# Optimization experiments

Measured on AMD Instinct MI355X. Metric: run time of the kernel, lower is better.

The kernel has to match this reference:

```python
import jax, jax.numpy as jnp
import numpy as np

DOF = 7
B = 8192
DT = 0.1
ACTION_RANGE = 50.0
MAX_VEL = 20.0


def _skew(w):
    x, y, z = w[..., 0], w[..., 1], w[..., 2]
    O = jnp.zeros_like(x)
    return jnp.stack([jnp.stack([O, -z, y], -1),
                      jnp.stack([z, O, -x], -1),
                      jnp.stack([-y, x, O], -1)], -2)


def _exp_se3(xi):
    # xi: (..., 6) twist [w; v] (already scaled by joint angle) -> (..., 4, 4)
    w, v = xi[..., :3], xi[..., 3:]
    th = jnp.sqrt(jnp.sum(w * w, -1))
    small = th < 1e-4
    ths = jnp.where(small, 1.0, th)  # safe denominator
    th2 = th * th
    a = jnp.where(small, 1.0 - th2 / 6.0, jnp.sin(th) / ths)
    b = jnp.where(small, 0.5 - th2 / 24.0, (1.0 - jnp.cos(th)) / (ths * ths))
    c = jnp.where(small, 1.0 / 6.0 - th2 / 120.0, (th - jnp.sin(th)) / (ths * ths * ths))
    K = _skew(w)
    K2 = K @ K
    I3 = jnp.eye(3, dtype=xi.dtype)
    R = I3 + a[..., None, None] * K + b[..., None, None] * K2
    Vm = I3 + b[..., None, None] * K + c[..., None, None] * K2
    p = jnp.einsum('...ij,...j->...i', Vm, v)
    top = jnp.concatenate([R, p[..., None]], -1)
    bot = jnp.broadcast_to(jnp.array([0.0, 0.0, 0.0, 1.0], xi.dtype), top.shape[:-2] + (1, 4))
    return jnp.concatenate([top, bot], -2)


def _inv_T(T):
    R = T[..., :3, :3]
    p = T[..., :3, 3]
    Rt = jnp.swapaxes(R, -1, -2)
    pn = -jnp.einsum('...ij,...j->...i', Rt, p)
    top = jnp.concatenate([Rt, pn[..., None]], -1)
    bot = jnp.broadcast_to(jnp.array([0.0, 0.0, 0.0, 1.0], T.dtype), top.shape[:-2] + (1, 4))
    return jnp.concatenate([top, bot], -2)


def _adjoint(T):
    # SE(3) adjoint for [w; v] twists: [[R, 0], [ [p]x R, R ]]
    R = T[..., :3, :3]
    p = T[..., :3, 3]
    pR = _skew(p) @ R
    Z = jnp.zeros_like(R)
    return jnp.concatenate([jnp.concatenate([R, Z], -1),
                            jnp.concatenate([pR, R], -1)], -2)


def _ad(V):
    # se(3) little adjoint: [[ [w]x, 0 ], [ [v]x, [w]x ]]
    Kw = _skew(V[..., :3])
    Kv = _skew(V[..., 3:])
    Z = jnp.zeros_like(Kw)
    return jnp.concatenate([jnp.concatenate([Kw, Z], -1),
                            jnp.concatenate([Kv, Kw], -1)], -2)


def _inverse_dynamics(q, dq, ddq, g, Ftip, M, G, A):
    # Recursive Newton-Euler (Modern Robotics, link-frame screws A).
    Bq, n = q.shape
    V = jnp.zeros((Bq, 6), q.dtype)
    Vd = jnp.broadcast_to(jnp.concatenate([jnp.zeros(3, q.dtype), -g]), (Bq, 6))
    AdTs, Vs, Vds = [], [], []
    for i in range(n):
        T = _exp_se3(-A[i] * q[:, i, None]) @ _inv_T(M[i])  # T_{i,i-1}, (B,4,4)
        AdT = _adjoint(T)
        V = jnp.einsum('bij,bj->bi', AdT, V) + A[i] * dq[:, i, None]
        Vd = (jnp.einsum('bij,bj->bi', AdT, Vd)
              + jnp.einsum('bij,j->bi', _ad(V), A[i]) * dq[:, i, None]
              + A[i] * ddq[:, i, None])
        AdTs.append(AdT)
        Vs.append(V)
        Vds.append(Vd)
    F = jnp.broadcast_to(Ftip.astype(q.dtype), (Bq, 6))
    AdT_end = _adjoint(_inv_T(M[n]))  # T_{n+1,n}, (6,6)
    taus = [None] * n
    for i in range(n - 1, -1, -1):
        if i == n - 1:
            F = jnp.einsum('ji,bj->bi', AdT_end, F)
        else:
            F = jnp.einsum('bji,bj->bi', AdTs[i + 1], F)
        F = (F + jnp.einsum('ij,bj->bi', G[i], Vds[i])
             - jnp.einsum('bji,jk,bk->bi', _ad(Vs[i]), G[i], Vs[i]))
        taus[i] = jnp.einsum('bi,i->b', F, A[i])
    return jnp.stack(taus, -1)  # (B, n)


def _forward_dynamics(q, dq, tau, g, Ftip, M, G, A):
    n = q.shape[1]
    zer = jnp.zeros_like(q)
    # bias forces: Coriolis + gravity + end-effector wrench
    h = _inverse_dynamics(q, dq, zer, g, Ftip, M, G, A)
    g0 = jnp.zeros(3, q.dtype)
    f0 = jnp.zeros(6, q.dtype)
    # mass matrix columns via unit accelerations (vmapped over columns)
    cols = jax.vmap(lambda e: _inverse_dynamics(
        q, zer, jnp.broadcast_to(e, q.shape), g0, f0, M, G, A))(jnp.eye(n, dtype=q.dtype))
    Mmat = jnp.transpose(cols, (1, 2, 0))  # (B, n, n)
    return jnp.linalg.solve(Mmat, (tau - h)[..., None])[..., 0]


def _fk_in_space(q, M, A):
    Bq, n = q.shape
    T = jnp.broadcast_to(jnp.eye(4, dtype=q.dtype), (Bq, 4, 4))
    outs = []
    for i in range(n):
        T = (T @ M[i]) @ _exp_se3(A[i] * q[:, i, None])
        outs.append(T)
    outs.append(T @ M[n])
    return jnp.stack(outs, 1)  # (B, n+1, 4, 4)


def setup_inputs():
    key = jax.random.key(0)
    ks = jax.random.split(key, 4)
    state = jax.random.normal(ks[0], (B, 2 * DOF), jnp.float32)
    torque = jax.random.normal(ks[1], (B, DOF), jnp.float32)
    M = jnp.tile(jnp.eye(4, dtype=jnp.float32)[None], (DOF + 1, 1, 1))
    A = jax.random.uniform(ks[2], (DOF, 6), jnp.float32)
    L = jax.random.normal(ks[3], (DOF, 6, 6), jnp.float32)
    gravity = jnp.array([0.0, -9.8, 0.0], jnp.float32)
    ftip = jnp.zeros(6, jnp.float32)
    return {"state": state, "torque": torque, "M": M, "A": A, "L": L,
            "gravity": gravity, "ftip": ftip}


def reference(state, torque, M, A, L, gravity, ftip):
    n = DOF
    G = L @ jnp.swapaxes(L, -1, -2)  # spatial inertias, PSD
    s0 = jnp.concatenate([state, torque * ACTION_RANGE], -1)  # (B, 3n)

    def derivs(s):
        q = s[..., :n]
        dq = s[..., n:2 * n]
        qf = s[..., 2 * n:]
        qacc = _forward_dynamics(q, dq, qf, gravity, ftip, M, G, A)
        return jnp.concatenate([dq, qacc, jnp.zeros_like(qf)], -1)

    k1 = derivs(s0)
    k2 = derivs(s0 + 0.5 * DT * k1)
    k3 = derivs(s0 + 0.5 * DT * k2)
    k4 = derivs(s0 + DT * k3)
    s1 = s0 + (DT / 6.0) * (k1 + 2.0 * k2 + 2.0 * k3 + k4)
    q = jnp.mod(s1[..., :n] + jnp.pi, 2.0 * jnp.pi) - jnp.pi
    dq = jnp.clip(s1[..., n:2 * n], -MAX_VEL, MAX_VEL)
    ee = _fk_in_space(q, M, A)
    return jnp.concatenate([q, dq], -1), ee[:, -1, :2, 3]
```

## Files before the change

kernel.cpp:

```cpp
#include <hip/hip_runtime.h>
#include <hip/hip_bf16.h>

#define DTC 0.1f
#define ACTION_RANGE 50.0f
#define MAX_VEL 20.0f
#define PI_F 3.14159265358979323846f
#define TWO_PI_F 6.28318530717958647692f
#define INV_TWO_PI_F 0.15915494309189533577f

__device__ __forceinline__ float bf2f(__hip_bfloat16 x){ return __bfloat162float(x); }
__device__ __forceinline__ float frcp(float x){ return __builtin_amdgcn_rcpf(x); }

__device__ __forceinline__ float ldv(const void* p, int i, bool isb){
  return isb ? __bfloat162float(((const __hip_bfloat16*)p)[i]) : ((const float*)p)[i];
}
__device__ __forceinline__ void stv(void* p, int i, float v, bool isb){
  if (isb) ((__hip_bfloat16*)p)[i] = __float2bfloat16(v);
  else     ((float*)p)[i] = v;
}

__device__ __forceinline__ void exp_se3_Rp(const float* Aj, float s, float* R, float* P){
  float wx=Aj[0]*s, wy=Aj[1]*s, wz=Aj[2]*s;
  float vx=Aj[3]*s, vy=Aj[4]*s, vz=Aj[5]*s;
  float th2 = wx*wx+wy*wy+wz*wz;
  float th = sqrtf(th2);
  float th4 = th2*th2;
  float aS = 1.f - th2*(1.f/6.f)  + th4*(1.f/120.f);
  float bS = 0.5f - th2*(1.f/24.f) + th4*(1.f/720.f);
  float cS = (1.f/6.f) - th2*(1.f/120.f) + th4*(1.f/5040.f);
  float sn = __sinf(th), cs = __cosf(th);
  float inv = frcp(th), inv2 = inv*inv;
  float aL = sn*inv;
  float bL = (1.f-cs)*inv2;
  float cL = (th-sn)*inv2*inv;
  bool sm = th < 0.25f;
  float a = sm?aS:aL, b = sm?bS:bL, c = sm?cS:cL;
  R[0]=1.f+b*(wx*wx-th2); R[1]=b*wx*wy-a*wz;      R[2]=b*wx*wz+a*wy;
  R[3]=b*wx*wy+a*wz;      R[4]=1.f+b*(wy*wy-th2); R[5]=b*wy*wz-a*wx;
  R[6]=b*wx*wz-a*wy;      R[7]=b*wy*wz+a*wx;      R[8]=1.f+b*(wz*wz-th2);
  float V0=1.f+c*(wx*wx-th2), V1=c*wx*wy-b*wz,      V2=c*wx*wz+b*wy;
  float V3=c*wx*wy+b*wz,      V4=1.f+c*(wy*wy-th2), V5=c*wy*wz-b*wx;
  float V6=c*wx*wz-b*wy,      V7=c*wy*wz+b*wx,      V8=1.f+c*(wz*wz-th2);
  P[0]=V0*vx+V1*vy+V2*vz;
  P[1]=V3*vx+V4*vy+V5*vz;
  P[2]=V6*vx+V7*vy+V8*vz;
}

__device__ __forceinline__ void mul33(const float* X, const float* Y, float* Z){
  #pragma unroll
  for (int r=0;r<3;r++){
    float x0=X[r*3+0], x1=X[r*3+1], x2=X[r*3+2];
    Z[r*3+0]=x0*Y[0]+x1*Y[3]+x2*Y[6];
    Z[r*3+1]=x0*Y[1]+x1*Y[4]+x2*Y[7];
    Z[r*3+2]=x0*Y[2]+x1*Y[5]+x2*Y[8];
  }
}

__device__ __forceinline__ void ad_apply(const float* R, const float* p, const float* Vin, float* Vout){
  float i0=Vin[0],i1=Vin[1],i2=Vin[2],i3=Vin[3],i4=Vin[4],i5=Vin[5];
  float w0 = R[0]*i0+R[1]*i1+R[2]*i2;
  float w1 = R[3]*i0+R[4]*i1+R[5]*i2;
  float w2 = R[6]*i0+R[7]*i1+R[8]*i2;
  float r0 = R[0]*i3+R[1]*i4+R[2]*i5;
  float r1 = R[3]*i3+R[4]*i4+R[5]*i5;
  float r2 = R[6]*i3+R[7]*i4+R[8]*i5;
  float p0=p[0],p1=p[1],p2=p[2];
  Vout[0]=w0; Vout[1]=w1; Vout[2]=w2;
  Vout[3]=p1*w2-p2*w1+r0;
  Vout[4]=p2*w0-p0*w2+r1;
  Vout[5]=p0*w1-p1*w0+r2;
}

__device__ __forceinline__ void adT_apply(const float* R, const float* p, const float* Fin, float* Fout){
  float m0=Fin[0],m1=Fin[1],m2=Fin[2],f0=Fin[3],f1=Fin[4],f2=Fin[5];
  float p0=p[0],p1=p[1],p2=p[2];
  float cx = m0 - (p1*f2 - p2*f1);
  float cy = m1 - (p2*f0 - p0*f2);
  float cz = m2 - (p0*f1 - p1*f0);
  float o0 = R[0]*cx + R[3]*cy + R[6]*cz;
  float o1 = R[1]*cx + R[4]*cy + R[7]*cz;
  float o2 = R[2]*cx + R[5]*cy + R[8]*cz;
  float o3 = R[0]*f0 + R[3]*f1 + R[6]*f2;
  float o4 = R[1]*f0 + R[4]*f1 + R[7]*f2;
  float o5 = R[2]*f0 + R[5]*f1 + R[8]*f2;
  Fout[0]=o0;Fout[1]=o1;Fout[2]=o2;Fout[3]=o3;Fout[4]=o4;Fout[5]=o5;
}

__device__ __forceinline__ void gmatvec2_sym(const float* Gu, const float* v, const float* d,
                                             float* gv, float* gvd){
  float g0=Gu[0],g1=Gu[1],g2=Gu[2],g3=Gu[3],g4=Gu[4],g5=Gu[5];
  float g6=Gu[6],g7=Gu[7],g8=Gu[8],g9=Gu[9],g10=Gu[10];
  float g11=Gu[11],g12=Gu[12],g13=Gu[13],g14=Gu[14];
  float g15=Gu[15],g16=Gu[16],g17=Gu[17],g18=Gu[18],g19=Gu[19],g20=Gu[20];
  gv[0]=g0*v[0]+g1 *v[1]+g2 *v[2]+g3 *v[3]+g4 *v[4]+g5 *v[5];
  gv[1]=g1*v[0]+g6 *v[1]+g7 *v[2]+g8 *v[3]+g9 *v[4]+g10*v[5];
  gv[2]=g2*v[0]+g7 *v[1]+g11*v[2]+g12*v[3]+g13*v[4]+g14*v[5];
  gv[3]=g3*v[0]+g8 *v[1]+g12*v[2]+g15*v[3]+g16*v[4]+g17*v[5];
  gv[4]=g4*v[0]+g9 *v[1]+g13*v[2]+g16*v[3]+g18*v[4]+g19*v[5];
  gv[5]=g5*v[0]+g10*v[1]+g14*v[2]+g17*v[3]+g19*v[4]+g20*v[5];
  gvd[0]=g0*d[0]+g1 *d[1]+g2 *d[2]+g3 *d[3]+g4 *d[4]+g5 *d[5];
  gvd[1]=g1*d[0]+g6 *d[1]+g7 *d[2]+g8 *d[3]+g9 *d[4]+g10*d[5];
  gvd[2]=g2*d[0]+g7 *d[1]+g11*d[2]+g12*d[3]+g13*d[4]+g14*d[5];
  gvd[3]=g3*d[0]+g8 *d[1]+g12*d[2]+g15*d[3]+g16*d[4]+g17*d[5];
  gvd[4]=g4*d[0]+g9 *d[1]+g13*d[2]+g16*d[3]+g18*d[4]+g19*d[5];
  gvd[5]=g5*d[0]+g10*d[1]+g14*d[2]+g17*d[3]+g19*d[4]+g20*d[5];
}

#define W_STRIDE 100

__global__ __launch_bounds__(64) void arm_rk4_kernel(
    const void* __restrict__ g_state,
    const void* __restrict__ g_torque,
    const void* __restrict__ g_M,
    const void* __restrict__ g_A,
    const void* __restrict__ g_L,
    const void* __restrict__ g_grav,
    const void* __restrict__ g_ftip,
    void* __restrict__ g_out,
    int B)
{
  __shared__ __align__(16) float sA8[56];
  __shared__ __align__(16) float sGu[168];
  __shared__ float sMinvR[72];
  __shared__ float sMinvp[24];
  __shared__ float sMR[72];
  __shared__ float sMp[24];
  __shared__ float sgrav[3];
  __shared__ float sftip[6];
  __shared__ __align__(16) float sW[8*W_STRIDE];
  __shared__ float sacc_lds[7*6*64];
  __shared__ float m_lds[7*64];
  __shared__ float dqs_lds[7*8];

  const bool isb = fabsf(bf2f(((const __hip_bfloat16*)g_grav)[1]) + 9.8f) < 0.5f;

  const int t = threadIdx.x;
  for (int x=t; x<56; x+=64){
    int i = x >> 3, k = x & 7;
    sA8[x] = (k < 6) ? ldv(g_A, i*6+k, isb) : 0.f;
  }
  for (int x=t; x<168; x+=64){
    int i = x/24; int u = x - i*24;
    if (u < 21){
      int rr = 0, u2 = u;
      while (u2 >= 6-rr){ u2 -= 6-rr; rr++; }
      int cc = rr + u2;
      float s = 0.f;
      #pragma unroll
      for (int k=0;k<6;k++) s += ldv(g_L, i*36+rr*6+k, isb) * ldv(g_L, i*36+cc*6+k, isb);
      sGu[x] = s;
    } else sGu[x] = 0.f;
  }
  if (t < 8){
    float R[9], p[3];
    #pragma unroll
    for (int rr=0;rr<3;rr++){
      #pragma unroll
      for (int cc=0;cc<3;cc++) R[rr*3+cc] = ldv(g_M, t*16 + rr*4 + cc, isb);
      p[rr] = ldv(g_M, t*16 + rr*4 + 3, isb);
    }
    #pragma unroll
    for (int rr=0;rr<3;rr++){
      #pragma unroll
      for (int cc=0;cc<3;cc++){ sMR[t*9+rr*3+cc] = R[rr*3+cc]; sMinvR[t*9+rr*3+cc] = R[cc*3+rr]; }
      sMp[t*3+rr] = p[rr];
      sMinvp[t*3+rr] = -(R[0*3+rr]*p[0] + R[1*3+rr]*p[1] + R[2*3+rr]*p[2]);
    }
  }
  if (t == 0){ for (int k=0;k<3;k++) sgrav[k] = ldv(g_grav, k, isb); }
  if (t == 1){ for (int k=0;k<6;k++) sftip[k] = ldv(g_ftip, k, isb); }
  __syncthreads();

  const int e = t >> 3;
  const int r = t & 7;
  int b = blockIdx.x * 8 + e;
  if (b >= B) b = B - 1;
  const bool is7 = (r == 7);
  float* W = &sW[e*W_STRIDE];

  float q0[7], dq0[7], qf[7];
  #pragma unroll
  for (int i=0;i<7;i++){
    q0[i]  = ldv(g_state, b*14+i, isb);
    dq0[i] = ldv(g_state, b*14+7+i, isb);
    qf[i]  = ldv(g_torque, b*7+i, isb) * ACTION_RANGE;
  }
  float kq[7], kdd[7], accq[7], accdq[7];
  #pragma unroll
  for (int i=0;i<7;i++){ kq[i]=0.f; kdd[i]=0.f; accq[i]=0.f; accdq[i]=0.f; }

  float Fend[6];
  {
    float tf[6]; adT_apply(&sMinvR[63], &sMinvp[21], sftip, tf);
    #pragma unroll
    for (int k=0;k<6;k++) Fend[k] = is7 ? tf[k] : 0.f;
  }

  #pragma unroll 1
  for (int st=0; st<4; ++st){
    const float cin = (st==0) ? 0.f : ((st==3) ? DTC : 0.5f*DTC);
    const float wgt = (st==0||st==3) ? (DTC/6.f) : (DTC/3.f);
    float qs[7], dqs[7];
    #pragma unroll
    for (int i=0;i<7;i++){ qs[i]=q0[i]+cin*kq[i]; dqs[i]=dq0[i]+cin*kdd[i]; }

    float qsr = 0.f;
    #pragma unroll
    for (int c=0;c<7;c++) qsr = (r==c) ? qs[c] : qsr;

    if (is7){
      #pragma unroll
      for (int i=0;i<7;i++) dqs_lds[i*8+e] = dqs[i];
    }

    if (r < 7){
      float Re[9], Pe[3], Rt[9];
      exp_se3_Rp(&sA8[r*8], -qsr, Re, Pe);
      mul33(Re, &sMinvR[r*9], Rt);
      float Tw[12];
      #pragma unroll
      for (int k=0;k<9;k++) Tw[k] = Rt[k];
      #pragma unroll
      for (int rr=0;rr<3;rr++)
        Tw[9+rr] = Re[rr*3+0]*sMinvp[r*3+0] + Re[rr*3+1]*sMinvp[r*3+1]
                 + Re[rr*3+2]*sMinvp[r*3+2] + Pe[rr];
      #pragma unroll
      for (int k=0;k<12;k++) W[r*12+k] = Tw[k];
    }
    __syncthreads();

    float V[6] = {0,0,0,0,0,0};
    float Vd[6];
    Vd[0]=0.f; Vd[1]=0.f; Vd[2]=0.f;
    Vd[3] = is7 ? -sgrav[0] : 0.f;
    Vd[4] = is7 ? -sgrav[1] : 0.f;
    Vd[5] = is7 ? -sgrav[2] : 0.f;
    #pragma unroll 1
    for (int i=0;i<7;i++){
      float Tl[12];
      #pragma unroll
      for (int k=0;k<12;k++) Tl[k] = W[i*12+k];
      float Al[6];
      #pragma unroll
      for (int k=0;k<6;k++) Al[k] = sA8[i*8+k];
      float dqi  = is7 ? dqs_lds[i*8+e] : 0.f;
      float ddqi = (!is7 && r==i) ? 1.f : 0.f;
      ad_apply(Tl, Tl+9, V, V);
      #pragma unroll
      for (int k=0;k<6;k++) V[k] += Al[k]*dqi;
      ad_apply(Tl, Tl+9, Vd, Vd);
      {
        float w0=V[0],w1=V[1],w2=V[2],v0=V[3],v1=V[4],v2=V[5];
        Vd[0] += (w1*Al[2]-w2*Al[1])*dqi + Al[0]*ddqi;
        Vd[1] += (w2*Al[0]-w0*Al[2])*dqi + Al[1]*ddqi;
        Vd[2] += (w0*Al[1]-w1*Al[0])*dqi + Al[2]*ddqi;
        Vd[3] += ((v1*Al[2]-v2*Al[1])+(w1*Al[5]-w2*Al[4]))*dqi + Al[3]*ddqi;
        Vd[4] += ((v2*Al[0]-v0*Al[2])+(w2*Al[3]-w0*Al[5]))*dqi + Al[4]*ddqi;
        Vd[5] += ((v0*Al[1]-v1*Al[0])+(w0*Al[4]-w1*Al[3]))*dqi + Al[5]*ddqi;
      }
      float gv[6], gvd[6];
      gmatvec2_sym(&sGu[i*24], V, Vd, gv, gvd);
      {
        float w0=V[0],w1=V[1],w2=V[2],v0=V[3],v1=V[4],v2=V[5];
        float s0 = gvd[0] + (w1*gv[2]-w2*gv[1]) + (v1*gv[5]-v2*gv[4]);
        float s1 = gvd[1] + (w2*gv[0]-w0*gv[2]) + (v2*gv[3]-v0*gv[5]);
        float s2 = gvd[2] + (w0*gv[1]-w1*gv[0]) + (v0*gv[4]-v1*gv[3]);
        float s3 = gvd[3] + (w1*gv[5]-w2*gv[4]);
        float s4 = gvd[4] + (w2*gv[3]-w0*gv[5]);
        float s5 = gvd[5] + (w0*gv[4]-w1*gv[3]);
        sacc_lds[(i*6+0)*64+t] = s0;
        sacc_lds[(i*6+1)*64+t] = s1;
        sacc_lds[(i*6+2)*64+t] = s2;
        sacc_lds[(i*6+3)*64+t] = s3;
        sacc_lds[(i*6+4)*64+t] = s4;
        sacc_lds[(i*6+5)*64+t] = s5;
      }
    }
    __syncthreads();

    {
      float F[6];
      #pragma unroll
      for (int k=0;k<6;k++) F[k] = Fend[k];
      #pragma unroll 1
      for (int i=6;i>=0;i--){
        if (i<6){
          float Tl[12];
          #pragma unroll
          for (int k=0;k<12;k++) Tl[k] = W[(i+1)*12+k];
          adT_apply(Tl, Tl+9, F, F);
        }
        #pragma unroll
        for (int k=0;k<6;k++) F[k] += sacc_lds[(i*6+k)*64+t];
        float Al[6];
        #pragma unroll
        for (int k=0;k<6;k++) Al[k] = sA8[i*8+k];
        m_lds[i*64+t] = F[0]*Al[0]+F[1]*Al[1]+F[2]*Al[2]
                      + F[3]*Al[3]+F[4]*Al[4]+F[5]*Al[5];
      }
    }
    __syncthreads();

    float U[7][7];
    #pragma unroll
    for (int i=0;i<7;i++){
      #pragma unroll
      for (int j=i;j<7;j++) U[i][j] = m_lds[j*64 + e*8 + i];
    }
    float rv[7];
    #pragma unroll
    for (int i=0;i<7;i++) rv[i] = qf[i] - m_lds[i*64 + e*8 + 7];
    #pragma unroll
    for (int k=0;k<7;k++){
      float dinv = frcp(U[k][k]);
      #pragma unroll
      for (int i=k+1;i<7;i++){
        float f = U[k][i]*dinv;
        #pragma unroll
        for (int j=i;j<7;j++) U[i][j] -= f*U[k][j];
        rv[i] -= f*rv[k];
      }
    }
    float x[7];
    #pragma unroll
    for (int i=6;i>=0;i--){
      float s = rv[i];
      #pragma unroll
      for (int j=i+1;j<7;j++) s -= U[i][j]*x[j];
      x[i] = s*frcp(U[i][i]);
    }

    #pragma unroll
    for (int i=0;i<7;i++){
      kq[i]  = dqs[i];
      kdd[i] = x[i];
      accq[i]  += wgt*dqs[i];
      accdq[i] += wgt*x[i];
    }
    __syncthreads();
  }

  float q1r=0.f, dq1r=0.f;
  #pragma unroll
  for (int c=0;c<7;c++){
    float xx = q0[c] + accq[c] + PI_F;
    float mm = xx - floorf(xx * INV_TWO_PI_F) * TWO_PI_F;
    float qv = mm - PI_F;
    float dv = dq0[c] + accdq[c];
    dv = fminf(fmaxf(dv, -MAX_VEL), MAX_VEL);
    q1r  = (r==c) ? qv : q1r;
    dq1r = (r==c) ? dv : dq1r;
  }

  {
    float XR[9], Xp[3];
    if (r < 7){
      float Re[9], Pe[3];
      exp_se3_Rp(&sA8[r*8], q1r, Re, Pe);
      mul33(&sMR[r*9], Re, XR);
      #pragma unroll
      for (int rr=0;rr<3;rr++)
        Xp[rr] = sMR[r*9+rr*3+0]*Pe[0]+sMR[r*9+rr*3+1]*Pe[1]+sMR[r*9+rr*3+2]*Pe[2] + sMp[r*3+rr];
    } else {
      #pragma unroll
      for (int k=0;k<9;k++) XR[k] = sMR[63+k];
      #pragma unroll
      for (int k=0;k<3;k++) Xp[k] = sMp[21+k];
    }
    #pragma unroll
    for (int k=0;k<9;k++) W[r*12+k]   = XR[k];
    #pragma unroll
    for (int k=0;k<3;k++) W[r*12+9+k] = Xp[k];
  }
  __syncthreads();

  #pragma unroll
  for (int w=4; w>=1; w>>=1){
    float Ra[9], pa[3], Rb[9], pb[3];
    if (r < w){
      #pragma unroll
      for (int k=0;k<9;k++){ Ra[k]=W[(2*r)*12+k]; Rb[k]=W[(2*r+1)*12+k]; }
      #pragma unroll
      for (int k=0;k<3;k++){ pa[k]=W[(2*r)*12+9+k]; pb[k]=W[(2*r+1)*12+9+k]; }
    }
    __syncthreads();
    if (r < w){
      float Rc[9];
      mul33(Ra, Rb, Rc);
      #pragma unroll
      for (int k=0;k<9;k++) W[r*12+k] = Rc[k];
      #pragma unroll
      for (int rr=0;rr<3;rr++)
        W[r*12+9+rr] = Ra[rr*3+0]*pb[0]+Ra[rr*3+1]*pb[1]+Ra[rr*3+2]*pb[2] + pa[rr];
    }
    __syncthreads();
  }

  if (r < 7){
    stv(g_out, b*14+r,   q1r,  isb);
    stv(g_out, b*14+7+r, dq1r, isb);
  } else {
    stv(g_out, B*14 + b*2 + 0, W[9],  isb);
    stv(g_out, B*14 + b*2 + 1, W[10], isb);
  }
}

extern "C" void kernel_launch(void* const* d_in, const int* in_sizes, int n_in,
                              void* d_out, int out_size, void* d_ws, size_t ws_size,
                              hipStream_t stream) {
  const int B = in_sizes[0] / 14;
  const int blocks = (B + 7) / 8;
  arm_rk4_kernel<<<blocks, 64, 0, stream>>>(d_in[0], d_in[1], d_in[2], d_in[3],
                                            d_in[4], d_in[5], d_in[6], d_out, B);
}
```

Baseline: 96.47 us.

## Keep per-lane RK4 state in scalars, drop redundant barriers, unroll RNEA loops

Each lane now carries only its own joint's q, dq, stage derivative and RK4 accumulators as scalars instead of full 7-element arrays. Only the is7 lane keeps a 7-wide copy of the previous solution, which it needs to publish dqs to LDS. The change also removes the barrier between the forward and backward Newton-Euler passes, since each thread reads back its own sacc entries, and removes the barrier at the end of each RK stage. The forward and backward link loops are unrolled by two. The aim is to cut register pressure, select chains and barrier stalls. The risk is that the barrier removal depends on subtle LDS ordering between stages.

```diff
diff --git a/kernel.cpp b/kernel.cpp
--- a/kernel.cpp
+++ b/kernel.cpp
@@ -178,16 +178,22 @@
   const bool is7 = (r == 7);
   float* W = &sW[e*W_STRIDE];
 
-  float q0[7], dq0[7], qf[7];
+  float dq0[7], qf[7];
   #pragma unroll
   for (int i=0;i<7;i++){
-    q0[i]  = ldv(g_state, b*14+i, isb);
     dq0[i] = ldv(g_state, b*14+7+i, isb);
     qf[i]  = ldv(g_torque, b*7+i, isb) * ACTION_RANGE;
   }
-  float kq[7], kdd[7], accq[7], accdq[7];
+  float q0r = ldv(g_state, b*14 + (is7 ? 0 : r), isb);
+  float dq0r = 0.f;
   #pragma unroll
-  for (int i=0;i<7;i++){ kq[i]=0.f; kdd[i]=0.f; accq[i]=0.f; accdq[i]=0.f; }
+  for (int c=0;c<7;c++) dq0r = (r==c) ? dq0[c] : dq0r;
+
+  float px[7];
+  #pragma unroll
+  for (int i=0;i<7;i++) px[i] = 0.f;
+  float pxr = 0.f, pdqr = 0.f;
+  float accq_r = 0.f, accdq_r = 0.f;
 
   float Fend[6];
   {
@@ -200,17 +206,12 @@
   for (int st=0; st<4; ++st){
     const float cin = (st==0) ? 0.f : ((st==3) ? DTC : 0.5f*DTC);
     const float wgt = (st==0||st==3) ? (DTC/6.f) : (DTC/3.f);
-    float qs[7], dqs[7];
-    #pragma unroll
-    for (int i=0;i<7;i++){ qs[i]=q0[i]+cin*kq[i]; dqs[i]=dq0[i]+cin*kdd[i]; }
-
-    float qsr = 0.f;
-    #pragma unroll
-    for (int c=0;c<7;c++) qsr = (r==c) ? qs[c] : qsr;
+    const float dqsr = dq0r + cin*pxr;
+    const float qsr  = q0r  + cin*pdqr;
 
     if (is7){
       #pragma unroll
-      for (int i=0;i<7;i++) dqs_lds[i*8+e] = dqs[i];
+      for (int i=0;i<7;i++) dqs_lds[i*8+e] = dq0[i] + cin*px[i];
     }
 
     if (r < 7){
@@ -235,7 +236,7 @@
     Vd[3] = is7 ? -sgrav[0] : 0.f;
     Vd[4] = is7 ? -sgrav[1] : 0.f;
     Vd[5] = is7 ? -sgrav[2] : 0.f;
-    #pragma unroll 1
+    #pragma unroll 2
     for (int i=0;i<7;i++){
       float Tl[12];
       #pragma unroll
@@ -262,27 +263,20 @@
       gmatvec2_sym(&sGu[i*24], V, Vd, gv, gvd);
       {
         float w0=V[0],w1=V[1],w2=V[2],v0=V[3],v1=V[4],v2=V[5];
-        float s0 = gvd[0] + (w1*gv[2]-w2*gv[1]) + (v1*gv[5]-v2*gv[4]);
-        float s1 = gvd[1] + (w2*gv[0]-w0*gv[2]) + (v2*gv[3]-v0*gv[5]);
-        float s2 = gvd[2] + (w0*gv[1]-w1*gv[0]) + (v0*gv[4]-v1*gv[3]);
-        float s3 = gvd[3] + (w1*gv[5]-w2*gv[4]);
-        float s4 = gvd[4] + (w2*gv[3]-w0*gv[5]);
-        float s5 = gvd[5] + (w0*gv[4]-w1*gv[3]);
-        sacc_lds[(i*6+0)*64+t] = s0;
-        sacc_lds[(i*6+1)*64+t] = s1;
-        sacc_lds[(i*6+2)*64+t] = s2;
-        sacc_lds[(i*6+3)*64+t] = s3;
-        sacc_lds[(i*6+4)*64+t] = s4;
-        sacc_lds[(i*6+5)*64+t] = s5;
+        sacc_lds[(i*6+0)*64+t] = gvd[0] + (w1*gv[2]-w2*gv[1]) + (v1*gv[5]-v2*gv[4]);
+        sacc_lds[(i*6+1)*64+t] = gvd[1] + (w2*gv[0]-w0*gv[2]) + (v2*gv[3]-v0*gv[5]);
+        sacc_lds[(i*6+2)*64+t] = gvd[2] + (w0*gv[1]-w1*gv[0]) + (v0*gv[4]-v1*gv[3]);
+        sacc_lds[(i*6+3)*64+t] = gvd[3] + (w1*gv[5]-w2*gv[4]);
+        sacc_lds[(i*6+4)*64+t] = gvd[4] + (w2*gv[3]-w0*gv[5]);
+        sacc_lds[(i*6+5)*64+t] = gvd[5] + (w0*gv[4]-w1*gv[3]);
       }
     }
-    __syncthreads();
 
     {
       float F[6];
       #pragma unroll
       for (int k=0;k<6;k++) F[k] = Fend[k];
-      #pragma unroll 1
+      #pragma unroll 2
       for (int i=6;i>=0;i--){
         if (i<6){
           float Tl[12];
@@ -330,26 +324,24 @@
       x[i] = s*frcp(U[i][i]);
     }
 
-    #pragma unroll
-    for (int i=0;i<7;i++){
-      kq[i]  = dqs[i];
-      kdd[i] = x[i];
-      accq[i]  += wgt*dqs[i];
-      accdq[i] += wgt*x[i];
-    }
-    __syncthreads();
-  }
-
-  float q1r=0.f, dq1r=0.f;
-  #pragma unroll
-  for (int c=0;c<7;c++){
-    float xx = q0[c] + accq[c] + PI_F;
+    float xr = 0.f;
+    #pragma unroll
+    for (int c=0;c<7;c++) xr = (r==c) ? x[c] : xr;
+    accq_r  += wgt*dqsr;
+    accdq_r += wgt*xr;
+    pdqr = dqsr;
+    pxr  = xr;
+    #pragma unroll
+    for (int i=0;i<7;i++) px[i] = x[i];
+  }
+
+  float q1r, dq1r;
+  {
+    float xx = q0r + accq_r + PI_F;
     float mm = xx - floorf(xx * INV_TWO_PI_F) * TWO_PI_F;
-    float qv = mm - PI_F;
-    float dv = dq0[c] + accdq[c];
-    dv = fminf(fmaxf(dv, -MAX_VEL), MAX_VEL);
-    q1r  = (r==c) ? qv : q1r;
-    dq1r = (r==c) ? dv : dq1r;
+    q1r = mm - PI_F;
+    float dv = dq0r + accdq_r;
+    dq1r = fminf(fmaxf(dv, -MAX_VEL), MAX_VEL);
   }
 
   {
```

Measured after the change: 95.12 us. About the same (-1.4%).
